# Performance work log

Measured on AMD Instinct MI355X. Metric: run time of the kernel, lower is better.

Reference implementation:

```python
import jax, jax.numpy as jnp
import numpy as np

N = 16384
E = 262144
IN_F, HID, ENC = 3, 128, 768
NEG_SLOPE = 0.2
EPS = 1e-5


def _glorot(key, shape):
    lim = float(np.sqrt(6.0 / (shape[0] + shape[1])))
    return jax.random.uniform(key, shape, jnp.float32, -lim, lim)


def layernorm(x, g, b):
    mu = jnp.mean(x, axis=-1, keepdims=True)
    var = jnp.mean(jnp.square(x - mu), axis=-1, keepdims=True)
    return (x - mu) * jax.lax.rsqrt(var + EPS) * g + b


def gatv2(x, src, dst, Wl, bl, Wr, br, att, bias, n_nodes):
    # single-head GATv2: message = lin_l(x)[src], score from lin_l(x)[src] + lin_r(x)[dst]
    xl = x @ Wl + bl                                  # [N, C]
    xr = x @ Wr + br                                  # [N, C]
    e = jax.nn.leaky_relu(xl[src] + xr[dst], NEG_SLOPE) @ att   # [E]
    m = jax.ops.segment_max(e, dst, num_segments=n_nodes)       # per-dst max (self-loops => no empty segs)
    ex = jnp.exp(e - m[dst])
    denom = jax.ops.segment_sum(ex, dst, num_segments=n_nodes)
    alpha = ex / denom[dst]                           # [E]
    out = jax.ops.segment_sum(alpha[:, None] * xl[src], dst, num_segments=n_nodes)
    return out + bias


def setup_inputs() -> dict:
    key = jax.random.key(0)
    ks = jax.random.split(key, 12)
    x = jax.random.normal(ks[0], (N, IN_F), jnp.float32)
    edge_index = jax.random.randint(ks[1], (2, E), 0, N, jnp.int64)
    return {
        "x": x,
        "edge_index": edge_index,
        "Wfc": _glorot(ks[2], (IN_F, ENC)),
        "bfc": jnp.zeros((ENC,), jnp.float32),
        "W1l": _glorot(ks[3], (IN_F, HID)),
        "b1l": jnp.zeros((HID,), jnp.float32),
        "W1r": _glorot(ks[4], (IN_F, HID)),
        "b1r": jnp.zeros((HID,), jnp.float32),
        "att1": _glorot(ks[5], (HID, 1))[:, 0],
        "bias1": jnp.zeros((HID,), jnp.float32),
        "g_bn1": jnp.ones((HID,), jnp.float32),
        "bb_bn1": jnp.zeros((HID,), jnp.float32),
        "W2l": _glorot(ks[6], (HID, ENC)),
        "b2l": jnp.zeros((ENC,), jnp.float32),
        "W2r": _glorot(ks[7], (HID, ENC)),
        "b2r": jnp.zeros((ENC,), jnp.float32),
        "att2": _glorot(ks[8], (ENC, 1))[:, 0],
        "bias2": jnp.zeros((ENC,), jnp.float32),
        "g_norm": jnp.ones((ENC,), jnp.float32),
        "b_norm": jnp.zeros((ENC,), jnp.float32),
    }


def reference(x, edge_index, Wfc, bfc, W1l, b1l, W1r, b1r, att1, bias1,
              g_bn1, bb_bn1, W2l, b2l, W2r, b2r, att2, bias2, g_norm, b_norm):
    loops = jnp.arange(N, dtype=edge_index.dtype)
    src = jnp.concatenate([edge_index[0], loops])   # add self-loops (PyG default)
    dst = jnp.concatenate([edge_index[1], loops])
    res = x @ Wfc + bfc                              # [N, ENC]
    h = gatv2(x, src, dst, W1l, b1l, W1r, b1r, att1, bias1, N)
    h = jax.nn.elu(layernorm(h, g_bn1, bb_bn1))
    h = gatv2(h, src, dst, W2l, b2l, W2r, b2r, att2, bias2, N)
    return layernorm(h + res, g_norm, b_norm)
```

## Files before the change

### kernel.cpp

```cpp
#include <hip/hip_runtime.h>

#define N_NODES 16384
#define N_EDGES 262144
#define EP (N_EDGES + N_NODES)
#define HID 128
#define ENC 768
#define ENCP (ENC/2)
#define EPSV 1e-5f

typedef unsigned short u16;
typedef unsigned char u8;
using f32x4  = __attribute__((ext_vector_type(4))) float;
using bf16x8 = __attribute__((ext_vector_type(8))) short;
using v2f    = __attribute__((ext_vector_type(2))) float;

__device__ __forceinline__ float wave_sum(float v){
  #pragma unroll
  for(int m=32;m>=1;m>>=1) v += __shfl_xor(v, m, 64);
  return v;
}
__device__ __forceinline__ unsigned bf16rtne(float f){
  const unsigned u = __float_as_uint(f);
  return (u + 0x7fffu + ((u>>16)&1u)) >> 16;
}
__device__ __forceinline__ unsigned pack2(float a, float b){
  return bf16rtne(a) | (bf16rtne(b) << 16);
}
__device__ __forceinline__ float bf2f(u16 h){ return __uint_as_float(((unsigned)h) << 16); }
__device__ __forceinline__ float plo(unsigned u){ return __uint_as_float(u << 16); }
__device__ __forceinline__ float phi(unsigned u){ return __uint_as_float(u & 0xffff0000u); }
__device__ __forceinline__ u8 f2fp8(float v){
  return (u8)(__builtin_amdgcn_cvt_pk_fp8_f32(v, v, 0, false) & 0xff);
}

#define Q4(ax, j, q) { \
  const v2f f01 = __builtin_amdgcn_cvt_pk_f32_fp8(ax, false); \
  const v2f f23 = __builtin_amdgcn_cvt_pk_f32_fp8(ax, true);  \
  q = fmaf(sg[j],   __builtin_fabsf(f01.x+xr[j]),   q); \
  q = fmaf(sg[j+1], __builtin_fabsf(f01.y+xr[j+1]), q); \
  q = fmaf(sg[j+2], __builtin_fabsf(f23.x+xr[j+2]), q); \
  q = fmaf(sg[j+3], __builtin_fabsf(f23.y+xr[j+3]), q); }

#define LIN1_BLKS (N_NODES/4)
#define WPREP_BLKS (2*ENC*HID/256)
#define HIST_BLKS (EP/256)
#define W2A_BLKS 258
__global__ __launch_bounds__(256) void prep_kernel(
    const float* __restrict__ x,
    const float* __restrict__ W1l, const float* __restrict__ b1l,
    const float* __restrict__ W1r, const float* __restrict__ b1r,
    const float* __restrict__ att1,
    const float* __restrict__ W2l, const float* __restrict__ W2r,
    const float* __restrict__ b2l, const float* __restrict__ b2r,
    const float* __restrict__ att2,
    const int* __restrict__ ei,
    unsigned* __restrict__ xl1p, unsigned* __restrict__ xr1p,
    float* __restrict__ dotl1, float* __restrict__ dotr1,
    u16* __restrict__ Wtb, float* __restrict__ w2a,
    int* __restrict__ hist){
  const int bid = blockIdx.x;
  if(bid < LIN1_BLKS){
    const int lane = threadIdx.x & 63;
    const int n = bid*4 + (threadIdx.x >> 6);
    const float x0 = x[n*3], x1 = x[n*3+1], x2 = x[n*3+2];
    const int c0 = lane, c1 = lane + 64;
    const float la = x0*W1l[c0] + x1*W1l[HID+c0] + x2*W1l[2*HID+c0] + b1l[c0];
    const float lb = x0*W1l[c1] + x1*W1l[HID+c1] + x2*W1l[2*HID+c1] + b1l[c1];
    const float ra = x0*W1r[c0] + x1*W1r[HID+c0] + x2*W1r[2*HID+c0] + b1r[c0];
    const float rb = x0*W1r[c1] + x1*W1r[HID+c1] + x2*W1r[2*HID+c1] + b1r[c1];
    const float aa = att1[c0], ab = att1[c1];
    const float dl = wave_sum(la*aa + lb*ab);
    const float dr = wave_sum(ra*aa + rb*ab);
    if(lane == 0){ dotl1[n] = 0.6f*dl; dotr1[n] = 0.6f*dr; }
    xl1p[n*64+lane] = pack2(la, lb);
    xr1p[n*64+lane] = pack2(ra, rb);
  } else if(bid < LIN1_BLKS + WPREP_BLKS){
    const int idx = (bid - LIN1_BLKS)*256 + threadIdx.x;
    const int n = idx >> 7, k = idx & 127;
    const float v = (n < ENC) ? W2l[k*ENC + n] : W2r[k*ENC + (n-ENC)];
    Wtb[idx] = (u16)bf16rtne(v);
  } else if(bid < LIN1_BLKS + WPREP_BLKS + HIST_BLKS){
    const int i = (bid - LIN1_BLKS - WPREP_BLKS)*256 + threadIdx.x;
    const int dst = (i < N_EDGES) ? ei[N_EDGES + i] : (i - N_EDGES);
    atomicAdd(&hist[dst], 1);
  } else {
    const int idx = bid - (LIN1_BLKS + WPREP_BLKS + HIST_BLKS);
    const float* src = (idx < 128) ? (W2l + (size_t)idx*ENC)
                     : (idx < 256) ? (W2r + (size_t)(idx-128)*ENC)
                     : (idx == 256) ? b2l : b2r;
    float partial = 0.f;
    for(int c = threadIdx.x; c < ENC; c += 256) partial += src[c]*att2[c];
    partial = wave_sum(partial);
    __shared__ float red4[4];
    if((threadIdx.x & 63) == 0) red4[threadIdx.x >> 6] = partial;
    __syncthreads();
    if(threadIdx.x == 0) w2a[idx] = red4[0]+red4[1]+red4[2]+red4[3];
  }
}

__global__ __launch_bounds__(1024) void scan_kernel(
    const int* __restrict__ hist, int* __restrict__ rowstart){
  __shared__ int sums[1024];
  const int t = threadIdx.x;
  const int base = t*16;
  int loc[16];
  int s = 0;
  #pragma unroll
  for(int i=0;i<16;i++){ loc[i] = s; s += hist[base+i]; }
  sums[t] = s;
  __syncthreads();
  for(int off=1; off<1024; off<<=1){
    int v = 0;
    if(t >= off) v = sums[t-off];
    __syncthreads();
    if(t >= off) sums[t] += v;
    __syncthreads();
  }
  const int prev = (t==0) ? 0 : sums[t-1];
  #pragma unroll
  for(int i=0;i<16;i++) rowstart[base+i] = prev + loc[i];
  if(t == 1023) rowstart[N_NODES] = EP;
}

__global__ __launch_bounds__(256) void scatter_kernel(
    const int* __restrict__ ei, const int* __restrict__ rowstart,
    int* __restrict__ cursor, int* __restrict__ ssrc){
  const int i = blockIdx.x*256 + threadIdx.x;
  const int src = (i < N_EDGES) ? ei[i]           : (i - N_EDGES);
  const int dst = (i < N_EDGES) ? ei[N_EDGES + i] : (i - N_EDGES);
  const int pos = rowstart[dst] + atomicAdd(&cursor[dst], 1);
  ssrc[pos] = src;
}

__global__ __launch_bounds__(256) void node1_kernel(
    const unsigned* __restrict__ xl1p, const unsigned* __restrict__ xr1p,
    const float* __restrict__ att1,
    const float* __restrict__ dotl1, const float* __restrict__ dotr1,
    const float* __restrict__ bias1,
    const float* __restrict__ g1, const float* __restrict__ b1,
    const float* __restrict__ w2a,
    const int* __restrict__ rowstart, const int* __restrict__ ssrc,
    u16* __restrict__ h1b, unsigned* __restrict__ h1p,
    float* __restrict__ dotl2, float* __restrict__ dotr2){
  const int lane = threadIdx.x & 63;
  const int n = blockIdx.x*4 + (threadIdx.x >> 6);
  const unsigned xru = xr1p[n*64 + lane];
  const float xra = plo(xru), xrb = phi(xru);
  const float sa = 0.4f*att1[lane], sb = 0.4f*att1[lane+64];
  const float ebase = dotr1[n];
  float acc0 = 0.f, acc1 = 0.f, denom = 0.f;
  int p = rowstart[n];
  const int p1 = rowstart[n+1];
  for(; p+3 < p1; p += 4){
    const int s0 = ssrc[p],   s1 = ssrc[p+1];
    const int s2 = ssrc[p+2], s3 = ssrc[p+3];
    const unsigned u0 = xl1p[s0*64 + lane];
    const unsigned u1 = xl1p[s1*64 + lane];
    const unsigned u2 = xl1p[s2*64 + lane];
    const unsigned u3 = xl1p[s3*64 + lane];
    const float dl0 = dotl1[s0], dl1 = dotl1[s1];
    const float dl2 = dotl1[s2], dl3 = dotl1[s3];
    const float a0 = plo(u0), b0 = phi(u0);
    const float a1 = plo(u1), b1v = phi(u1);
    const float a2 = plo(u2), b2v = phi(u2);
    const float a3 = plo(u3), b3v = phi(u3);
    float q0 = fmaf(sa, __builtin_fabsf(a0+xra), sb*__builtin_fabsf(b0+xrb));
    float q1 = fmaf(sa, __builtin_fabsf(a1+xra), sb*__builtin_fabsf(b1v+xrb));
    float q2 = fmaf(sa, __builtin_fabsf(a2+xra), sb*__builtin_fabsf(b2v+xrb));
    float q3 = fmaf(sa, __builtin_fabsf(a3+xra), sb*__builtin_fabsf(b3v+xrb));
    #pragma unroll
    for(int m=32;m>=1;m>>=1){
      q0 += __shfl_xor(q0, m, 64);
      q1 += __shfl_xor(q1, m, 64);
      q2 += __shfl_xor(q2, m, 64);
      q3 += __shfl_xor(q3, m, 64);
    }
    const float w0 = __expf(q0 + dl0 + ebase), w1 = __expf(q1 + dl1 + ebase);
    const float w2 = __expf(q2 + dl2 + ebase), w3 = __expf(q3 + dl3 + ebase);
    denom += (w0+w1) + (w2+w3);
    acc0 += w0*a0 + w1*a1 + w2*a2 + w3*a3;
    acc1 += w0*b0 + w1*b1v + w2*b2v + w3*b3v;
  }
  for(; p < p1; ++p){
    const int s0 = ssrc[p];
    const unsigned u0 = xl1p[s0*64 + lane];
    const float a0 = plo(u0), b0 = phi(u0);
    const float q = wave_sum(fmaf(sa, __builtin_fabsf(a0+xra), sb*__builtin_fabsf(b0+xrb)));
    const float w0 = __expf(q + dotl1[s0] + ebase);
    denom += w0; acc0 += w0*a0; acc1 += w0*b0;
  }
  const float inv = 1.f/denom;
  const float y0 = acc0*inv + bias1[lane];
  const float y1 = acc1*inv + bias1[lane+64];
  const float mu  = wave_sum(y0+y1) * (1.f/HID);
  const float d0 = y0-mu, d1 = y1-mu;
  const float var = wave_sum(d0*d0 + d1*d1) * (1.f/HID);
  const float r = rsqrtf(var + EPSV);
  float z0 = d0*r*g1[lane] + b1[lane];
  float z1 = d1*r*g1[lane+64] + b1[lane+64];
  z0 = z0 > 0.f ? z0 : expm1f(z0);
  z1 = z1 > 0.f ? z1 : expm1f(z1);
  h1b[n*HID+lane]    = (u16)bf16rtne(z0);
  h1b[n*HID+lane+64] = (u16)bf16rtne(z1);
  h1p[n*64+lane]     = pack2(z0, z1);
  float dl2 = z0*w2a[lane]     + z1*w2a[lane+64];
  float dr2 = z0*w2a[128+lane] + z1*w2a[128+lane+64];
  #pragma unroll
  for(int m=32;m>=1;m>>=1){
    dl2 += __shfl_xor(dl2, m, 64);
    dr2 += __shfl_xor(dr2, m, 64);
  }
  if(lane == 0){
    dotl2[n] = 0.6f*(dl2 + w2a[256]);
    dotr2[n] = 0.6f*(dr2 + w2a[257]);
  }
}

#define LBM 128
#define LBN 128
__global__ __launch_bounds__(256) void mfma_lin2_kernel(
    const u16* __restrict__ h1b, const u16* __restrict__ Wtb,
    const float* __restrict__ b2l, const float* __restrict__ b2r,
    u8* __restrict__ xl8, u16* __restrict__ xr2u){
  __shared__ __align__(16) u16 Cs[LBM*128];
  const int t = threadIdx.x;
  const int mb = blockIdx.x * LBM;
  const int nb = blockIdx.y * LBN;
  const int w = t >> 6, lane = t & 63;
  const int l15 = lane & 15, g = lane >> 4;
  const int ar0 = mb + w*32 + l15, ar1 = ar0 + 16;
  bf16x8 a0[4], a1[4];
  #pragma unroll
  for(int ks=0;ks<4;ks++){
    a0[ks] = *(const bf16x8*)(h1b + (size_t)ar0*128 + ks*32 + g*8);
    a1[ks] = *(const bf16x8*)(h1b + (size_t)ar1*128 + ks*32 + g*8);
  }
  f32x4 acc0[8], acc1[8];
  #pragma unroll
  for(int j=0;j<8;j++){ acc0[j]=(f32x4){0,0,0,0}; acc1[j]=(f32x4){0,0,0,0}; }
  #pragma unroll
  for(int j=0;j<8;j++){
    const int brn = nb + j*16 + l15;
    #pragma unroll
    for(int ks=0;ks<4;ks++){
      const bf16x8 b = *(const bf16x8*)(Wtb + (size_t)brn*128 + ks*32 + g*8);
      acc0[j] = __builtin_amdgcn_mfma_f32_16x16x32_bf16(a0[ks], b, acc0[j], 0,0,0);
      acc1[j] = __builtin_amdgcn_mfma_f32_16x16x32_bf16(a1[ks], b, acc1[j], 0,0,0);
    }
  }
  if(nb < ENC){
    u8* Cs8 = (u8*)Cs;
    float biasj[8];
    #pragma unroll
    for(int j=0;j<8;j++) biasj[j] = b2l[nb + j*16 + l15];
    #pragma unroll
    for(int j=0;j<8;j++){
      const int col = j*16 + l15;
      #pragma unroll
      for(int r4=0;r4<4;r4++){
        const int row0 = w*32 + g*4 + r4;
        Cs8[row0*128 + (col ^ ((row0&7)<<4))] = f2fp8(acc0[j][r4] + biasj[j]);
        const int row1 = row0 + 16;
        Cs8[row1*128 + (col ^ ((row1&7)<<4))] = f2fp8(acc1[j][r4] + biasj[j]);
      }
    }
    __syncthreads();
    #pragma unroll
    for(int idx=t; idx<LBM*8; idx+=256){
      const int row = idx >> 3, ch = idx & 7;
      const uint4 v = *(const uint4*)(Cs8 + row*128 + ((ch*16) ^ ((row&7)<<4)));
      *(uint4*)(xl8 + (size_t)(mb+row)*ENC + nb + ch*16) = v;
    }
  } else {
    const float* bsrc = b2r + (nb - ENC);
    float biasj[8];
    #pragma unroll
    for(int j=0;j<8;j++) biasj[j] = bsrc[j*16 + l15];
    #pragma unroll
    for(int j=0;j<8;j++){
      const int coll = j*16 + l15;
      #pragma unroll
      for(int r4=0;r4<4;r4++){
        const int row0 = w*32 + g*4 + r4;
        *(u16*)((char*)Cs + row0*256 + ((coll*2) ^ ((row0&7)<<4))) =
            (u16)bf16rtne(acc0[j][r4] + biasj[j]);
        const int row1 = row0 + 16;
        *(u16*)((char*)Cs + row1*256 + ((coll*2) ^ ((row1&7)<<4))) =
            (u16)bf16rtne(acc1[j][r4] + biasj[j]);
      }
    }
    __syncthreads();
    u16* dst0 = xr2u + (nb - ENC);
    const int rr = t >> 4, cc = t & 15;
    #pragma unroll
    for(int it=0; it<8; ++it){
      const int row = it*16 + rr;
      const uint4 v = *(const uint4*)((const char*)Cs + row*256 + ((cc*16) ^ ((row&7)<<4)));
      *(uint4*)(dst0 + (size_t)(mb+row)*ENC + cc*8) = v;
    }
  }
}

__global__ __launch_bounds__(256) void node2b_kernel(
    const u8* __restrict__ xl8, const u8* __restrict__ xr2u8,
    const float* __restrict__ att2,
    const float* __restrict__ dotl2, const float* __restrict__ dotr2,
    const unsigned* __restrict__ h1p,
    const int* __restrict__ rowstart, const int* __restrict__ ssrc,
    u16* __restrict__ aggb){
  const int lane = threadIdx.x & 63;
  const int n = blockIdx.x*4 + (threadIdx.x >> 6);
  float sg[12], xr[12];
  {
    const float4* A4 = (const float4*)(att2 + lane*12);
    const float4 s0 = A4[0], s1 = A4[1], s2 = A4[2];
    sg[0]=0.4f*s0.x; sg[1]=0.4f*s0.y; sg[2]=0.4f*s0.z; sg[3]=0.4f*s0.w;
    sg[4]=0.4f*s1.x; sg[5]=0.4f*s1.y; sg[6]=0.4f*s1.z; sg[7]=0.4f*s1.w;
    sg[8]=0.4f*s2.x; sg[9]=0.4f*s2.y; sg[10]=0.4f*s2.z; sg[11]=0.4f*s2.w;
    const u8* xrrow = xr2u8 + (size_t)n*(ENC*2) + lane*24;
    const uint2 r0 = *(const uint2*)(xrrow);
    const uint2 r1 = *(const uint2*)(xrrow + 8);
    const uint2 r2 = *(const uint2*)(xrrow + 16);
    xr[0]=plo(r0.x); xr[1]=phi(r0.x); xr[2]=plo(r0.y); xr[3]=phi(r0.y);
    xr[4]=plo(r1.x); xr[5]=phi(r1.x); xr[6]=plo(r1.y); xr[7]=phi(r1.y);
    xr[8]=plo(r2.x); xr[9]=phi(r2.x); xr[10]=plo(r2.y); xr[11]=phi(r2.y);
  }
  const float ebase = dotr2[n];
  float denom = 0.f, acc0 = 0.f, acc1 = 0.f;
  int p = rowstart[n];
  const int p1 = rowstart[n+1];
  for(; p+3 < p1; p += 4){
    const int s0 = ssrc[p],   s1 = ssrc[p+1];
    const int s2 = ssrc[p+2], s3 = ssrc[p+3];
    const uint3 a0 = *(const uint3*)(xl8 + (size_t)s0*ENC + lane*12);
    const uint3 a1 = *(const uint3*)(xl8 + (size_t)s1*ENC + lane*12);
    const uint3 a2 = *(const uint3*)(xl8 + (size_t)s2*ENC + lane*12);
    const uint3 a3 = *(const uint3*)(xl8 + (size_t)s3*ENC + lane*12);
    const float dl0 = dotl2[s0], dl1 = dotl2[s1];
    const float dl2 = dotl2[s2], dl3 = dotl2[s3];
    const unsigned h0 = h1p[s0*64 + lane];
    const unsigned h1 = h1p[s1*64 + lane];
    const unsigned h2 = h1p[s2*64 + lane];
    const unsigned h3 = h1p[s3*64 + lane];
    float q0 = 0.f, q1 = 0.f, q2 = 0.f, q3 = 0.f;
    Q4(a0.x, 0, q0) Q4(a0.y, 4, q0) Q4(a0.z, 8, q0)
    Q4(a1.x, 0, q1) Q4(a1.y, 4, q1) Q4(a1.z, 8, q1)
    Q4(a2.x, 0, q2) Q4(a2.y, 4, q2) Q4(a2.z, 8, q2)
    Q4(a3.x, 0, q3) Q4(a3.y, 4, q3) Q4(a3.z, 8, q3)
    #pragma unroll
    for(int m=32;m>=1;m>>=1){
      q0 += __shfl_xor(q0, m, 64);
      q1 += __shfl_xor(q1, m, 64);
      q2 += __shfl_xor(q2, m, 64);
      q3 += __shfl_xor(q3, m, 64);
    }
    const float w0 = __expf(q0 + dl0 + ebase), w1 = __expf(q1 + dl1 + ebase);
    const float w2 = __expf(q2 + dl2 + ebase), w3 = __expf(q3 + dl3 + ebase);
    denom += (w0+w1) + (w2+w3);
    acc0 += w0*plo(h0) + w1*plo(h1) + w2*plo(h2) + w3*plo(h3);
    acc1 += w0*phi(h0) + w1*phi(h1) + w2*phi(h2) + w3*phi(h3);
  }
  for(; p < p1; ++p){
    const int s0 = ssrc[p];
    const uint3 a0 = *(const uint3*)(xl8 + (size_t)s0*ENC + lane*12);
    float q0 = 0.f;
    Q4(a0.x, 0, q0) Q4(a0.y, 4, q0) Q4(a0.z, 8, q0)
    const unsigned h0 = h1p[s0*64 + lane];
    const float w0 = __expf(wave_sum(q0) + dotl2[s0] + ebase);
    denom += w0; acc0 += w0*plo(h0); acc1 += w0*phi(h0);
  }
  const float inv = 1.f/denom;
  aggb[n*HID+lane]    = (u16)bf16rtne(acc0*inv);
  aggb[n*HID+lane+64] = (u16)bf16rtne(acc1*inv);
}

#define YSTR 770
__global__ __launch_bounds__(256) void gemm3_mfma_kernel(
    const u16* __restrict__ aggb, const u16* __restrict__ Wtb,
    const float* __restrict__ b2l, const float* __restrict__ bias2,
    const float* __restrict__ x, const float* __restrict__ Wfc,
    const float* __restrict__ bfc,
    const float* __restrict__ gn, const float* __restrict__ bn,
    float* __restrict__ out){
  __shared__ u16 Ys[64*YSTR];
  __shared__ float cbs[ENC];
  __shared__ float wfs[3][ENC];
  __shared__ float mus[64], rss[64];
  const int t = threadIdx.x;
  const int mb = blockIdx.x * 64;
  for(int c=t; c<ENC; c+=256){
    cbs[c] = b2l[c] + bias2[c] + bfc[c];
    wfs[0][c] = Wfc[c]; wfs[1][c] = Wfc[ENC+c]; wfs[2][c] = Wfc[2*ENC+c];
  }
  const int w = t >> 6, lane = t & 63;
  const int l15 = lane & 15, g = lane >> 4;
  const int ar = mb + w*16 + l15;
  bf16x8 a[4];
  #pragma unroll
  for(int ks=0;ks<4;ks++)
    a[ks] = *(const bf16x8*)(aggb + (size_t)ar*128 + ks*32 + g*8);
  float xv0[4], xv1[4], xv2[4];
  #pragma unroll
  for(int r4=0;r4<4;r4++){
    const int rrow = mb + w*16 + g*4 + r4;
    xv0[r4] = x[rrow*3]; xv1[r4] = x[rrow*3+1]; xv2[r4] = x[rrow*3+2];
  }
  float rs[4] = {0,0,0,0}, rq[4] = {0,0,0,0};
  __syncthreads();
  #pragma unroll
  for(int sub=0; sub<6; ++sub){
    const int nb = sub*128;
    f32x4 acc[8];
    #pragma unroll
    for(int j=0;j<8;j++) acc[j]=(f32x4){0,0,0,0};
    #pragma unroll
    for(int j=0;j<8;j++){
      const int brn = nb + j*16 + l15;
      #pragma unroll
      for(int ks=0;ks<4;ks++){
        const bf16x8 b = *(const bf16x8*)(Wtb + (size_t)brn*128 + ks*32 + g*8);
        acc[j] = __builtin_amdgcn_mfma_f32_16x16x32_bf16(a[ks], b, acc[j], 0,0,0);
      }
    }
    #pragma unroll
    for(int j=0;j<8;j++){
      const int col = nb + j*16 + l15;
      const float cb = cbs[col];
      const float w0 = wfs[0][col], w1 = wfs[1][col], w2 = wfs[2][col];
      #pragma unroll
      for(int r4=0;r4<4;r4++){
        const int lrow = w*16 + g*4 + r4;
        const float y = acc[j][r4] + cb + xv0[r4]*w0 + xv1[r4]*w1 + xv2[r4]*w2;
        rs[r4] += y; rq[r4] += y*y;
        Ys[lrow*YSTR + col] = (u16)bf16rtne(y);
      }
    }
  }
  #pragma unroll
  for(int m=8;m>=1;m>>=1){
    #pragma unroll
    for(int r4=0;r4<4;r4++){
      rs[r4] += __shfl_xor(rs[r4], m, 64);
      rq[r4] += __shfl_xor(rq[r4], m, 64);
    }
  }
  if(l15 == 0){
    #pragma unroll
    for(int r4=0;r4<4;r4++){
      const int lrow = w*16 + g*4 + r4;
      const float mu = rs[r4] * (1.f/ENC);
      const float var = rq[r4] * (1.f/ENC) - mu*mu;
      mus[lrow] = mu;
      rss[lrow] = rsqrtf(var + EPSV);
    }
  }
  __syncthreads();
  float gv[12], bv[12];
  #pragma unroll
  for(int j2=0;j2<12;j2++){ gv[j2] = gn[lane + j2*64]; bv[j2] = bn[lane + j2*64]; }
  for(int r=0; r<16; ++r){
    const int lrow = w*16 + r;
    const float mu = mus[lrow], rstd = rss[lrow];
    float* orow = out + (size_t)(mb+lrow)*ENC;
    #pragma unroll
    for(int j2=0;j2<12;j2++){
      const float y = bf2f(Ys[lrow*YSTR + lane + j2*64]);
      orow[lane + j2*64] = (y - mu)*rstd*gv[j2] + bv[j2];
    }
  }
}

extern "C" void kernel_launch(void* const* d_in, const int* in_sizes, int n_in,
                              void* d_out, int out_size, void* d_ws, size_t ws_size,
                              hipStream_t stream) {
  const float* x    = (const float*)d_in[0];
  const int*   ei   = (const int*)  d_in[1];
  const float* Wfc  = (const float*)d_in[2];
  const float* bfc  = (const float*)d_in[3];
  const float* W1l  = (const float*)d_in[4];
  const float* b1l  = (const float*)d_in[5];
  const float* W1r  = (const float*)d_in[6];
  const float* b1r  = (const float*)d_in[7];
  const float* att1 = (const float*)d_in[8];
  const float* bias1= (const float*)d_in[9];
  const float* g1   = (const float*)d_in[10];
  const float* bb1  = (const float*)d_in[11];
  const float* W2l  = (const float*)d_in[12];
  const float* b2l  = (const float*)d_in[13];
  const float* W2r  = (const float*)d_in[14];
  const float* b2r  = (const float*)d_in[15];
  const float* att2 = (const float*)d_in[16];
  const float* bias2= (const float*)d_in[17];
  const float* gn   = (const float*)d_in[18];
  const float* bn   = (const float*)d_in[19];
  float* out = (float*)d_out;

  char* w = (char*)d_ws;
  auto alloc = [&](size_t bytes){ void* p = (void*)w; w += (bytes + 255) & ~(size_t)255; return p; };
  int*      hist     = (int*)     alloc((size_t)N_NODES*4);
  int*      cursor   = (int*)     alloc((size_t)N_NODES*4);
  int*      rowstart = (int*)     alloc((size_t)(N_NODES+1)*4);
  int*      ssrc     = (int*)     alloc((size_t)EP*4);
  unsigned* xl1p     = (unsigned*)alloc((size_t)N_NODES*64*4);
  unsigned* xr1p     = (unsigned*)alloc((size_t)N_NODES*64*4);
  float*    dotl1    = (float*)   alloc((size_t)N_NODES*4);
  float*    dotr1    = (float*)   alloc((size_t)N_NODES*4);
  float*    dotl2    = (float*)   alloc((size_t)N_NODES*4);
  float*    dotr2    = (float*)   alloc((size_t)N_NODES*4);
  u16*      h1b      = (u16*)     alloc((size_t)N_NODES*HID*2);
  unsigned* h1p      = (unsigned*)alloc((size_t)N_NODES*64*4);
  u16*      aggb     = (u16*)     alloc((size_t)N_NODES*HID*2);
  u8*       xl8      = (u8*)      alloc((size_t)N_NODES*ENC);
  u16*      xr2u     = (u16*)     alloc((size_t)N_NODES*ENC*2);
  u16*      Wtb      = (u16*)     alloc((size_t)2*ENC*HID*2);
  float*    w2a      = (float*)   alloc((size_t)W2A_BLKS*4);

  hipMemsetAsync(hist, 0, (size_t)N_NODES*8, stream);

  prep_kernel<<<LIN1_BLKS+WPREP_BLKS+HIST_BLKS+W2A_BLKS, 256, 0, stream>>>(
      x, W1l, b1l, W1r, b1r, att1, W2l, W2r, b2l, b2r, att2, ei,
      xl1p, xr1p, dotl1, dotr1, Wtb, w2a, hist);
  scan_kernel<<<1, 1024, 0, stream>>>(hist, rowstart);
  scatter_kernel<<<EP/256, 256, 0, stream>>>(ei, rowstart, cursor, ssrc);
  node1_kernel<<<N_NODES/4, 256, 0, stream>>>(xl1p, xr1p, att1, dotl1, dotr1,
                                              bias1, g1, bb1, w2a,
                                              rowstart, ssrc, h1b, h1p, dotl2, dotr2);
  mfma_lin2_kernel<<<dim3(N_NODES/LBM, 2*ENC/LBN), 256, 0, stream>>>(
      h1b, Wtb, b2l, b2r, xl8, xr2u);
  node2b_kernel<<<N_NODES/4, 256, 0, stream>>>(xl8, (const u8*)xr2u, att2,
                                               dotl2, dotr2, h1p,
                                               rowstart, ssrc, aggb);
  gemm3_mfma_kernel<<<N_NODES/64, 256, 0, stream>>>(aggb, Wtb, b2l, bias2,
                                                    x, Wfc, bfc, gn, bn, out);
}
```

Baseline: 190.2 us.

## Interleave hidden channels, process four edges per wave in node1, split node2 edges

Layer-1 features are now stored with channels interleaved (2*lane, 2*lane+1), so one packed bf16 buffer serves as both the per-node gather layout and the GEMM A operand, and the separate h1b buffer is dropped. node1 splits each wave into four 16-lane groups that each handle one edge using 128-bit loads and a 4-step shuffle reduction. Partial sums are combined across groups at the end, and the layernorm uses a one-pass E[x^2]-mu^2 variance. node2b now gives each node two waves that each take half its edge list, merging through shared memory to raise parallelism, at the cost of a block barrier and twice as many blocks.

```diff
diff --git a/kernel.cpp b/kernel.cpp
--- a/kernel.cpp
+++ b/kernel.cpp
@@ -5,7 +5,6 @@
 #define EP (N_EDGES + N_NODES)
 #define HID 128
 #define ENC 768
-#define ENCP (ENC/2)
 #define EPSV 1e-5f
 
 typedef unsigned short u16;
@@ -54,7 +53,7 @@
     const float* __restrict__ b2l, const float* __restrict__ b2r,
     const float* __restrict__ att2,
     const int* __restrict__ ei,
-    unsigned* __restrict__ xl1p, unsigned* __restrict__ xr1p,
+    unsigned* __restrict__ xl1u, unsigned* __restrict__ xr1u,
     float* __restrict__ dotl1, float* __restrict__ dotr1,
     u16* __restrict__ Wtb, float* __restrict__ w2a,
     int* __restrict__ hist){
@@ -63,7 +62,7 @@
     const int lane = threadIdx.x & 63;
     const int n = bid*4 + (threadIdx.x >> 6);
     const float x0 = x[n*3], x1 = x[n*3+1], x2 = x[n*3+2];
-    const int c0 = lane, c1 = lane + 64;
+    const int c0 = 2*lane, c1 = 2*lane + 1;
     const float la = x0*W1l[c0] + x1*W1l[HID+c0] + x2*W1l[2*HID+c0] + b1l[c0];
     const float lb = x0*W1l[c1] + x1*W1l[HID+c1] + x2*W1l[2*HID+c1] + b1l[c1];
     const float ra = x0*W1r[c0] + x1*W1r[HID+c0] + x2*W1r[2*HID+c0] + b1r[c0];
@@ -72,8 +71,8 @@
     const float dl = wave_sum(la*aa + lb*ab);
     const float dr = wave_sum(ra*aa + rb*ab);
     if(lane == 0){ dotl1[n] = 0.6f*dl; dotr1[n] = 0.6f*dr; }
-    xl1p[n*64+lane] = pack2(la, lb);
-    xr1p[n*64+lane] = pack2(ra, rb);
+    xl1u[n*64+lane] = pack2(la, lb);
+    xr1u[n*64+lane] = pack2(ra, rb);
   } else if(bid < LIN1_BLKS + WPREP_BLKS){
     const int idx = (bid - LIN1_BLKS)*256 + threadIdx.x;
     const int n = idx >> 7, k = idx & 127;
@@ -133,86 +132,101 @@
 }
 
 __global__ __launch_bounds__(256) void node1_kernel(
-    const unsigned* __restrict__ xl1p, const unsigned* __restrict__ xr1p,
+    const unsigned* __restrict__ xl1u, const unsigned* __restrict__ xr1u,
     const float* __restrict__ att1,
     const float* __restrict__ dotl1, const float* __restrict__ dotr1,
     const float* __restrict__ bias1,
     const float* __restrict__ g1, const float* __restrict__ b1,
     const float* __restrict__ w2a,
     const int* __restrict__ rowstart, const int* __restrict__ ssrc,
-    u16* __restrict__ h1b, unsigned* __restrict__ h1p,
+    unsigned* __restrict__ h1u,
     float* __restrict__ dotl2, float* __restrict__ dotr2){
   const int lane = threadIdx.x & 63;
   const int n = blockIdx.x*4 + (threadIdx.x >> 6);
-  const unsigned xru = xr1p[n*64 + lane];
-  const float xra = plo(xru), xrb = phi(xru);
-  const float sa = 0.4f*att1[lane], sb = 0.4f*att1[lane+64];
+  const int g = lane >> 4, k = lane & 15;
+  float xr[8], sa[8];
+  {
+    const uint4 u = *(const uint4*)(xr1u + n*64 + 4*k);
+    xr[0]=plo(u.x); xr[1]=phi(u.x); xr[2]=plo(u.y); xr[3]=phi(u.y);
+    xr[4]=plo(u.z); xr[5]=phi(u.z); xr[6]=plo(u.w); xr[7]=phi(u.w);
+    const float4 a0 = *(const float4*)(att1 + 8*k);
+    const float4 a1 = *(const float4*)(att1 + 8*k + 4);
+    sa[0]=0.4f*a0.x; sa[1]=0.4f*a0.y; sa[2]=0.4f*a0.z; sa[3]=0.4f*a0.w;
+    sa[4]=0.4f*a1.x; sa[5]=0.4f*a1.y; sa[6]=0.4f*a1.z; sa[7]=0.4f*a1.w;
+  }
   const float ebase = dotr1[n];
-  float acc0 = 0.f, acc1 = 0.f, denom = 0.f;
-  int p = rowstart[n];
-  const int p1 = rowstart[n+1];
-  for(; p+3 < p1; p += 4){
-    const int s0 = ssrc[p],   s1 = ssrc[p+1];
-    const int s2 = ssrc[p+2], s3 = ssrc[p+3];
-    const unsigned u0 = xl1p[s0*64 + lane];
-    const unsigned u1 = xl1p[s1*64 + lane];
-    const unsigned u2 = xl1p[s2*64 + lane];
-    const unsigned u3 = xl1p[s3*64 + lane];
-    const float dl0 = dotl1[s0], dl1 = dotl1[s1];
-    const float dl2 = dotl1[s2], dl3 = dotl1[s3];
-    const float a0 = plo(u0), b0 = phi(u0);
-    const float a1 = plo(u1), b1v = phi(u1);
-    const float a2 = plo(u2), b2v = phi(u2);
-    const float a3 = plo(u3), b3v = phi(u3);
-    float q0 = fmaf(sa, __builtin_fabsf(a0+xra), sb*__builtin_fabsf(b0+xrb));
-    float q1 = fmaf(sa, __builtin_fabsf(a1+xra), sb*__builtin_fabsf(b1v+xrb));
-    float q2 = fmaf(sa, __builtin_fabsf(a2+xra), sb*__builtin_fabsf(b2v+xrb));
-    float q3 = fmaf(sa, __builtin_fabsf(a3+xra), sb*__builtin_fabsf(b3v+xrb));
-    #pragma unroll
-    for(int m=32;m>=1;m>>=1){
-      q0 += __shfl_xor(q0, m, 64);
-      q1 += __shfl_xor(q1, m, 64);
-      q2 += __shfl_xor(q2, m, 64);
-      q3 += __shfl_xor(q3, m, 64);
-    }
-    const float w0 = __expf(q0 + dl0 + ebase), w1 = __expf(q1 + dl1 + ebase);
-    const float w2 = __expf(q2 + dl2 + ebase), w3 = __expf(q3 + dl3 + ebase);
-    denom += (w0+w1) + (w2+w3);
-    acc0 += w0*a0 + w1*a1 + w2*a2 + w3*a3;
-    acc1 += w0*b0 + w1*b1v + w2*b2v + w3*b3v;
-  }
-  for(; p < p1; ++p){
-    const int s0 = ssrc[p];
-    const unsigned u0 = xl1p[s0*64 + lane];
-    const float a0 = plo(u0), b0 = phi(u0);
-    const float q = wave_sum(fmaf(sa, __builtin_fabsf(a0+xra), sb*__builtin_fabsf(b0+xrb)));
-    const float w0 = __expf(q + dotl1[s0] + ebase);
-    denom += w0; acc0 += w0*a0; acc1 += w0*b0;
+  float acc[8] = {0,0,0,0,0,0,0,0};
+  float denom = 0.f;
+  const int p0 = rowstart[n], p1 = rowstart[n+1];
+  for(int base = p0; base < p1; base += 4){
+    const int idx = base + g;
+    const bool valid = idx < p1;
+    const int s = ssrc[valid ? idx : (p1-1)];
+    const uint4 u = *(const uint4*)(xl1u + s*64 + 4*k);
+    float a[8];
+    a[0]=plo(u.x); a[1]=phi(u.x); a[2]=plo(u.y); a[3]=phi(u.y);
+    a[4]=plo(u.z); a[5]=phi(u.z); a[6]=plo(u.w); a[7]=phi(u.w);
+    const float dlv = dotl1[s];
+    float q = 0.f;
+    #pragma unroll
+    for(int j=0;j<8;j++) q = fmaf(sa[j], __builtin_fabsf(a[j]+xr[j]), q);
+    q += __shfl_xor(q, 1, 64);
+    q += __shfl_xor(q, 2, 64);
+    q += __shfl_xor(q, 4, 64);
+    q += __shfl_xor(q, 8, 64);
+    float w = __expf(q + dlv + ebase);
+    w = valid ? w : 0.f;
+    denom += w;
+    #pragma unroll
+    for(int j=0;j<8;j++) acc[j] = fmaf(w, a[j], acc[j]);
+  }
+  #pragma unroll
+  for(int m=16; m<64; m<<=1){
+    denom += __shfl_xor(denom, m, 64);
+    #pragma unroll
+    for(int j=0;j<8;j++) acc[j] += __shfl_xor(acc[j], m, 64);
   }
   const float inv = 1.f/denom;
-  const float y0 = acc0*inv + bias1[lane];
-  const float y1 = acc1*inv + bias1[lane+64];
-  const float mu  = wave_sum(y0+y1) * (1.f/HID);
-  const float d0 = y0-mu, d1 = y1-mu;
-  const float var = wave_sum(d0*d0 + d1*d1) * (1.f/HID);
+  const float4 bb0 = *(const float4*)(bias1 + 8*k);
+  const float4 bb1 = *(const float4*)(bias1 + 8*k + 4);
+  float y[8];
+  y[0]=acc[0]*inv+bb0.x; y[1]=acc[1]*inv+bb0.y; y[2]=acc[2]*inv+bb0.z; y[3]=acc[3]*inv+bb0.w;
+  y[4]=acc[4]*inv+bb1.x; y[5]=acc[5]*inv+bb1.y; y[6]=acc[6]*inv+bb1.z; y[7]=acc[7]*inv+bb1.w;
+  float ls = 0.f, lq = 0.f;
+  #pragma unroll
+  for(int j=0;j<8;j++){ ls += y[j]; lq += y[j]*y[j]; }
+  ls = wave_sum(ls); lq = wave_sum(lq);
+  const float mu  = ls * (1.f/(4*HID));
+  const float var = lq * (1.f/(4*HID)) - mu*mu;
   const float r = rsqrtf(var + EPSV);
-  float z0 = d0*r*g1[lane] + b1[lane];
-  float z1 = d1*r*g1[lane+64] + b1[lane+64];
-  z0 = z0 > 0.f ? z0 : expm1f(z0);
-  z1 = z1 > 0.f ? z1 : expm1f(z1);
-  h1b[n*HID+lane]    = (u16)bf16rtne(z0);
-  h1b[n*HID+lane+64] = (u16)bf16rtne(z1);
-  h1p[n*64+lane]     = pack2(z0, z1);
-  float dl2 = z0*w2a[lane]     + z1*w2a[lane+64];
-  float dr2 = z0*w2a[128+lane] + z1*w2a[128+lane+64];
-  #pragma unroll
-  for(int m=32;m>=1;m>>=1){
-    dl2 += __shfl_xor(dl2, m, 64);
-    dr2 += __shfl_xor(dr2, m, 64);
-  }
+  const float4 gg0 = *(const float4*)(g1 + 8*k);
+  const float4 gg1 = *(const float4*)(g1 + 8*k + 4);
+  const float4 ob0 = *(const float4*)(b1 + 8*k);
+  const float4 ob1 = *(const float4*)(b1 + 8*k + 4);
+  const float gv[8] = {gg0.x,gg0.y,gg0.z,gg0.w,gg1.x,gg1.y,gg1.z,gg1.w};
+  const float bv[8] = {ob0.x,ob0.y,ob0.z,ob0.w,ob1.x,ob1.y,ob1.z,ob1.w};
+  float z[8];
+  #pragma unroll
+  for(int j=0;j<8;j++){
+    float zz = (y[j]-mu)*r*gv[j] + bv[j];
+    z[j] = zz > 0.f ? zz : expm1f(zz);
+  }
+  float dl2 = 0.f, dr2 = 0.f;
+  #pragma unroll
+  for(int j=0;j<8;j++){
+    dl2 = fmaf(z[j], w2a[8*k+j], dl2);
+    dr2 = fmaf(z[j], w2a[128+8*k+j], dr2);
+  }
+  dl2 = wave_sum(dl2); dr2 = wave_sum(dr2);
   if(lane == 0){
-    dotl2[n] = 0.6f*(dl2 + w2a[256]);
-    dotr2[n] = 0.6f*(dr2 + w2a[257]);
+    dotl2[n] = 0.6f*(0.25f*dl2 + w2a[256]);
+    dotr2[n] = 0.6f*(0.25f*dr2 + w2a[257]);
+  }
+  if(g == 0){
+    uint4 o;
+    o.x = pack2(z[0], z[1]); o.y = pack2(z[2], z[3]);
+    o.z = pack2(z[4], z[5]); o.w = pack2(z[6], z[7]);
+    *(uint4*)(h1u + n*64 + 4*k) = o;
   }
 }
 
@@ -305,11 +319,14 @@
     const u8* __restrict__ xl8, const u8* __restrict__ xr2u8,
     const float* __restrict__ att2,
     const float* __restrict__ dotl2, const float* __restrict__ dotr2,
-    const unsigned* __restrict__ h1p,
+    const unsigned* __restrict__ h1u,
     const int* __restrict__ rowstart, const int* __restrict__ ssrc,
-    u16* __restrict__ aggb){
+    unsigned* __restrict__ aggb){
+  __shared__ float comb[4][64][4];
   const int lane = threadIdx.x & 63;
-  const int n = blockIdx.x*4 + (threadIdx.x >> 6);
+  const int wid = threadIdx.x >> 6;
+  const int n = blockIdx.x*2 + (wid >> 1);
+  const int half = wid & 1;
   float sg[12], xr[12];
   {
     const float4* A4 = (const float4*)(att2 + lane*12);
@@ -327,9 +344,11 @@
   }
   const float ebase = dotr2[n];
   float denom = 0.f, acc0 = 0.f, acc1 = 0.f;
-  int p = rowstart[n];
-  const int p1 = rowstart[n+1];
-  for(; p+3 < p1; p += 4){
+  const int p0 = rowstart[n], p1v = rowstart[n+1];
+  const int mid = p0 + ((p1v - p0 + 1) >> 1);
+  int p = half ? mid : p0;
+  const int pe = half ? p1v : mid;
+  for(; p+3 < pe; p += 4){
     const int s0 = ssrc[p],   s1 = ssrc[p+1];
     const int s2 = ssrc[p+2], s3 = ssrc[p+3];
     const uint3 a0 = *(const uint3*)(xl8 + (size_t)s0*ENC + lane*12);
@@ -338,10 +357,10 @@
     const uint3 a3 = *(const uint3*)(xl8 + (size_t)s3*ENC + lane*12);
     const float dl0 = dotl2[s0], dl1 = dotl2[s1];
     const float dl2 = dotl2[s2], dl3 = dotl2[s3];
-    const unsigned h0 = h1p[s0*64 + lane];
-    const unsigned h1 = h1p[s1*64 + lane];
-    const unsigned h2 = h1p[s2*64 + lane];
-    const unsigned h3 = h1p[s3*64 + lane];
+    const unsigned h0 = h1u[s0*64 + lane];
+    const unsigned h1 = h1u[s1*64 + lane];
+    const unsigned h2 = h1u[s2*64 + lane];
+    const unsigned h3 = h1u[s3*64 + lane];
     float q0 = 0.f, q1 = 0.f, q2 = 0.f, q3 = 0.f;
     Q4(a0.x, 0, q0) Q4(a0.y, 4, q0) Q4(a0.z, 8, q0)
     Q4(a1.x, 0, q1) Q4(a1.y, 4, q1) Q4(a1.z, 8, q1)
@@ -360,18 +379,26 @@
     acc0 += w0*plo(h0) + w1*plo(h1) + w2*plo(h2) + w3*plo(h3);
     acc1 += w0*phi(h0) + w1*phi(h1) + w2*phi(h2) + w3*phi(h3);
   }
-  for(; p < p1; ++p){
+  for(; p < pe; ++p){
     const int s0 = ssrc[p];
     const uint3 a0 = *(const uint3*)(xl8 + (size_t)s0*ENC + lane*12);
     float q0 = 0.f;
     Q4(a0.x, 0, q0) Q4(a0.y, 4, q0) Q4(a0.z, 8, q0)
-    const unsigned h0 = h1p[s0*64 + lane];
+    const unsigned h0 = h1u[s0*64 + lane];
     const float w0 = __expf(wave_sum(q0) + dotl2[s0] + ebase);
     denom += w0; acc0 += w0*plo(h0); acc1 += w0*phi(h0);
   }
-  const float inv = 1.f/denom;
-  aggb[n*HID+lane]    = (u16)bf16rtne(acc0*inv);
-  aggb[n*HID+lane+64] = (u16)bf16rtne(acc1*inv);
+  comb[wid][lane][0] = denom;
+  comb[wid][lane][1] = acc0;
+  comb[wid][lane][2] = acc1;
+  __syncthreads();
+  if(half == 0){
+    denom += comb[wid+1][lane][0];
+    acc0  += comb[wid+1][lane][1];
+    acc1  += comb[wid+1][lane][2];
+    const float inv = 1.f/denom;
+    aggb[n*64 + lane] = pack2(acc0*inv, acc1*inv);
+  }
 }
 
 #define YSTR 770
@@ -501,15 +528,14 @@
   int*      cursor   = (int*)     alloc((size_t)N_NODES*4);
   int*      rowstart = (int*)     alloc((size_t)(N_NODES+1)*4);
   int*      ssrc     = (int*)     alloc((size_t)EP*4);
-  unsigned* xl1p     = (unsigned*)alloc((size_t)N_NODES*64*4);
-  unsigned* xr1p     = (unsigned*)alloc((size_t)N_NODES*64*4);
+  unsigned* xl1u     = (unsigned*)alloc((size_t)N_NODES*64*4);
+  unsigned* xr1u     = (unsigned*)alloc((size_t)N_NODES*64*4);
   float*    dotl1    = (float*)   alloc((size_t)N_NODES*4);
   float*    dotr1    = (float*)   alloc((size_t)N_NODES*4);
   float*    dotl2    = (float*)   alloc((size_t)N_NODES*4);
   float*    dotr2    = (float*)   alloc((size_t)N_NODES*4);
-  u16*      h1b      = (u16*)     alloc((size_t)N_NODES*HID*2);
-  unsigned* h1p      = (unsigned*)alloc((size_t)N_NODES*64*4);
-  u16*      aggb     = (u16*)     alloc((size_t)N_NODES*HID*2);
+  unsigned* h1u      = (unsigned*)alloc((size_t)N_NODES*64*4);
+  unsigned* aggb     = (unsigned*)alloc((size_t)N_NODES*64*4);
   u8*       xl8      = (u8*)      alloc((size_t)N_NODES*ENC);
   u16*      xr2u     = (u16*)     alloc((size_t)N_NODES*ENC*2);
   u16*      Wtb      = (u16*)     alloc((size_t)2*ENC*HID*2);
@@ -519,17 +545,17 @@
 
   prep_kernel<<<LIN1_BLKS+WPREP_BLKS+HIST_BLKS+W2A_BLKS, 256, 0, stream>>>(
       x, W1l, b1l, W1r, b1r, att1, W2l, W2r, b2l, b2r, att2, ei,
-      xl1p, xr1p, dotl1, dotr1, Wtb, w2a, hist);
+      xl1u, xr1u, dotl1, dotr1, Wtb, w2a, hist);
   scan_kernel<<<1, 1024, 0, stream>>>(hist, rowstart);
   scatter_kernel<<<EP/256, 256, 0, stream>>>(ei, rowstart, cursor, ssrc);
-  node1_kernel<<<N_NODES/4, 256, 0, stream>>>(xl1p, xr1p, att1, dotl1, dotr1,
+  node1_kernel<<<N_NODES/4, 256, 0, stream>>>(xl1u, xr1u, att1, dotl1, dotr1,
                                               bias1, g1, bb1, w2a,
-                                              rowstart, ssrc, h1b, h1p, dotl2, dotr2);
+                                              rowstart, ssrc, h1u, dotl2, dotr2);
   mfma_lin2_kernel<<<dim3(N_NODES/LBM, 2*ENC/LBN), 256, 0, stream>>>(
-      h1b, Wtb, b2l, b2r, xl8, xr2u);
-  node2b_kernel<<<N_NODES/4, 256, 0, stream>>>(xl8, (const u8*)xr2u, att2,
-                                               dotl2, dotr2, h1p,
+      (const u16*)h1u, Wtb, b2l, b2r, xl8, xr2u);
+  node2b_kernel<<<N_NODES/2, 256, 0, stream>>>(xl8, (const u8*)xr2u, att2,
+                                               dotl2, dotr2, h1u,
                                                rowstart, ssrc, aggb);
-  gemm3_mfma_kernel<<<N_NODES/64, 256, 0, stream>>>(aggb, Wtb, b2l, bias2,
+  gemm3_mfma_kernel<<<N_NODES/64, 256, 0, stream>>>((const u16*)aggb, Wtb, b2l, bias2,
                                                     x, Wfc, bfc, gn, bn, out);
 }
```

Measured after the change: 191.7 us. No clear change (+0.8%).
